# Kernel tuning notes

Measured on AMD Instinct MI355X. Metric: run time of the kernel, lower is better.

## Reference

```python
import jax, jax.numpy as jnp
import numpy as np
from jax import lax

SIM_THRESH = 0.9
MOTION_SCALE = 0.5
SALIENCY_SCALE = 0.5
EPS = 1e-6


def setup_inputs() -> dict:
    key = jax.random.key(0)
    k1, k2, k3, k4 = jax.random.split(key, 4)
    B, N, D, H, W = 128, 196, 768, 14, 14
    return {
        "tokens": jax.random.normal(k1, (B, N, D), dtype=jnp.float32),
        "motion_magnitude": jax.random.uniform(k2, (B, 1, H, W), dtype=jnp.float32),
        "saliency_map": jax.random.uniform(k3, (B, 1, H, W), dtype=jnp.float32),
        "compression_ratio": jax.random.uniform(k4, (B, H, W), dtype=jnp.float32),
    }


def _importance(motion, saliency, ratio):
    # motion/saliency are already (B,1,14,14) == (height,width), so
    # adaptive_avg_pool2d to (14,14) is the identity.
    B = motion.shape[0]
    m = motion.reshape(B, -1)
    m = m / (jnp.max(m) + EPS)               # global max, as in torch .max()
    s = saliency.reshape(B, -1)
    s = s / (jnp.max(s) + EPS)
    r = ratio.reshape(B, -1)
    imp = (MOTION_SCALE * m + SALIENCY_SCALE * s
           + (1.0 - MOTION_SCALE - SALIENCY_SCALE) * r)
    lo = imp.min(axis=1, keepdims=True)
    hi = imp.max(axis=1, keepdims=True)
    return (imp - lo) / (hi - lo + EPS)      # (B, N)


def _groups(adj):
    """Sequential BFS grouping over roots, faithful to the torch loop.

    adj: bool (N,N) directed edge mask. Returns (group_ids int32 (N,), num_groups).
    """
    N = adj.shape[0]

    def root_step(carry, r):
        assigned, gids, gid = carry

        def assign(c):
            assigned, gids, gid = c
            # BFS from root r, only through currently-unassigned nodes
            allowed = (~assigned).at[r].set(True)
            reach0 = jnp.zeros(N, dtype=bool).at[r].set(True)

            def body(s):
                reach, _ = s
                nxt = reach | (jnp.any(adj & reach[:, None], axis=0) & allowed)
                return nxt, jnp.any(nxt != reach)

            reach, _ = lax.while_loop(lambda s: s[1], body, (reach0, True))
            return assigned | reach, jnp.where(reach, gid, gids), gid + 1

        carry = lax.cond(assigned[r], lambda c: c, assign, carry)
        return carry, None

    init = (jnp.zeros(N, dtype=bool), jnp.zeros(N, dtype=jnp.int32), jnp.int32(0))
    (_, gids, ngroups), _ = lax.scan(root_step, init, jnp.arange(N))
    return gids, ngroups


def _merge_one(tokens_b, imp_b, adj_b):
    N = tokens_b.shape[0]
    gids, ng = _groups(adj_b)
    denom = jax.ops.segment_sum(imp_b, gids, num_segments=N) + EPS
    w = imp_b / denom[gids]
    merged = jax.ops.segment_sum(tokens_b * w[:, None], gids, num_segments=N)
    return merged, gids, ng


def reference(tokens, motion_magnitude, saliency_map, compression_ratio):
    B, N, D = tokens.shape
    imp = _importance(motion_magnitude, saliency_map, compression_ratio)  # (B,N)

    # cosine similarity (F.normalize with eps=1e-12)
    norm = jnp.maximum(jnp.linalg.norm(tokens, axis=-1, keepdims=True), 1e-12)
    tn = tokens / norm
    sim = jnp.einsum('bnd,bmd->bnm', tn, tn)
    sim = sim * (1.0 - jnp.eye(N, dtype=sim.dtype))  # zero diagonal

    # directed merge mask: similarity * (1 - importance_row)
    mask = (sim > SIM_THRESH).astype(sim.dtype) * (1.0 - imp[:, :, None])
    adj = mask > 0.5

    merged, gids, ng = jax.vmap(_merge_one)(tokens, imp, adj)
    # merged padded to N groups (rows >= num_groups are zero)
    return merged, sim, imp, gids
```

## Files before the change

### kernel.cpp

```cpp
#include <hip/hip_runtime.h>
#include <cstdint>

static constexpr int cB = 128;
static constexpr int cN = 196;
static constexpr int cD = 768;
static constexpr int cNN = cN * cN;
static constexpr int cND = cN * cD;
static constexpr float cEPS = 1e-6f;
static constexpr size_t cBND = (size_t)cB * cN * cD;

typedef __attribute__((ext_vector_type(8))) short short8;
typedef __attribute__((ext_vector_type(8))) unsigned short u16x8;
typedef __attribute__((ext_vector_type(4))) float f32x4;
typedef unsigned long long u64;

__device__ __forceinline__ unsigned short bf16_rne(float x) {
    unsigned u = __builtin_bit_cast(unsigned, x);
    u += 0x7FFFu + ((u >> 16) & 1u);
    return (unsigned short)(u >> 16);
}

__global__ __launch_bounds__(256) void k_imp(const float* __restrict__ mo,
                                             const float* __restrict__ sa,
                                             float* __restrict__ out_imp,
                                             float* __restrict__ ws_imp,
                                             float* __restrict__ ws_w,
                                             u64* __restrict__ ws_adj) {
    int b = blockIdx.x, t = threadIdx.x;
    __shared__ float redm[4], reds[4], lo_s[4], hi_s[4], MS[2], LOHI[2];

    for (int i = b * 256 + t; i < cB * cN * 4; i += cB * 256) ws_adj[i] = 0ull;

    const float4* mo4 = (const float4*)mo;
    const float4* sa4 = (const float4*)sa;
    float mm = 0.f, ms = 0.f;
    for (int i = t; i < cB * cN / 4; i += 256) {
        float4 a = mo4[i], c = sa4[i];
        mm = fmaxf(mm, fmaxf(fmaxf(a.x, a.y), fmaxf(a.z, a.w)));
        ms = fmaxf(ms, fmaxf(fmaxf(c.x, c.y), fmaxf(c.z, c.w)));
    }
    #pragma unroll
    for (int off = 32; off; off >>= 1) {
        mm = fmaxf(mm, __shfl_down(mm, off));
        ms = fmaxf(ms, __shfl_down(ms, off));
    }
    if ((t & 63) == 0) { redm[t >> 6] = mm; reds[t >> 6] = ms; }
    __syncthreads();
    if (t == 0) {
        float a = redm[0], c = reds[0];
        for (int w = 1; w < 4; w++) { a = fmaxf(a, redm[w]); c = fmaxf(c, reds[w]); }
        MS[0] = 1.0f / (a + cEPS);
        MS[1] = 1.0f / (c + cEPS);
    }
    __syncthreads();
    float Minv = MS[0], Sinv = MS[1];
    float v = 0.f, lo = 1e30f, hi = -1e30f;
    if (t < cN) {
        v = 0.5f * mo[b * cN + t] * Minv + 0.5f * sa[b * cN + t] * Sinv;
        lo = v; hi = v;
    }
    #pragma unroll
    for (int off = 32; off; off >>= 1) {
        lo = fminf(lo, __shfl_down(lo, off));
        hi = fmaxf(hi, __shfl_down(hi, off));
    }
    if ((t & 63) == 0) { lo_s[t >> 6] = lo; hi_s[t >> 6] = hi; }
    __syncthreads();
    if (t == 0) {
        float l = lo_s[0], h = hi_s[0];
        for (int w = 1; w < 4; w++) { l = fminf(l, lo_s[w]); h = fmaxf(h, hi_s[w]); }
        LOHI[0] = l; LOHI[1] = h;
    }
    __syncthreads();
    if (t < cN) {
        float imp = (v - LOHI[0]) / (LOHI[1] - LOHI[0] + cEPS);
        out_imp[b * cN + t] = imp;
        ws_imp[b * cN + t] = imp;
        ws_w[b * cN + t] = imp / (imp + cEPS);
    }
}

__global__ __launch_bounds__(256) void k_prep(const float* __restrict__ tok,
                                              const float* __restrict__ ws_w,
                                              float* __restrict__ ws_invn,
                                              float* __restrict__ merged) {
    int t = threadIdx.x;
    int tk = blockIdx.x * 8 + (t >> 5);
    int l  = t & 31;
    const float4* src = (const float4*)(tok + (size_t)tk * cD) + l;
    float4* dst = (float4*)(merged + (size_t)tk * cD) + l;
    float w = ws_w[tk];
    float4 v[6];
    #pragma unroll
    for (int j = 0; j < 6; j++) v[j] = src[32 * j];
    float s = 0.f;
    #pragma unroll
    for (int j = 0; j < 6; j++) {
        float4 x = v[j];
        s += x.x * x.x + x.y * x.y + x.z * x.z + x.w * x.w;
        dst[32 * j] = make_float4(x.x * w, x.y * w, x.z * w, x.w * w);
    }
    s += __shfl_xor(s, 1);  s += __shfl_xor(s, 2);
    s += __shfl_xor(s, 4);  s += __shfl_xor(s, 8);
    s += __shfl_xor(s, 16);
    if (l == 0) ws_invn[tk] = 1.0f / fmaxf(sqrtf(s), 1e-12f);
}

__global__ __launch_bounds__(256, 2) void k_sim(const float* __restrict__ tok,
                                                const float* __restrict__ ws_invn,
                                                const float* __restrict__ ws_imp,
                                                float* __restrict__ out_sim,
                                                u64* __restrict__ ws_adj) {
    __shared__ unsigned short sA[128 * 40];
    __shared__ unsigned short sB[128 * 40];
    __shared__ float invR[128], invC[128], impR[128];
    __shared__ u64 ldsAdj[256];

    int bid = blockIdx.x;
    int xcd = bid & 7;
    int lin = bid >> 3;
    int b   = xcd + 8 * (lin >> 2);
    int tile = lin & 3;
    int rb = (tile >> 1) * 128, cb = (tile & 1) * 128;

    int t = threadIdx.x;
    int w = t >> 6, lane = t & 63;
    int lr = lane & 15, kf = (lane >> 4) * 8;
    int wr = (w >> 1) * 64, wc = (w & 1) * 64;
    const size_t bN = (size_t)b * cN;
    const float* tb = tok + bN * cD;

    ldsAdj[t] = 0ull;
    if (t < 128) {
        int gr = rb + t;
        invR[t] = (gr < cN) ? ws_invn[bN + gr] : 0.f;
        impR[t] = (gr < cN) ? ws_imp[bN + gr] : 1.f;
    } else {
        int gc = cb + (t - 128);
        invC[t - 128] = (gc < cN) ? ws_invn[bN + gc] : 0.f;
    }

    f32x4 acc[4][4];
    #pragma unroll
    for (int i = 0; i < 4; i++)
        #pragma unroll
        for (int j = 0; j < 4; j++) acc[i][j] = (f32x4){0.f, 0.f, 0.f, 0.f};

    int srow = t >> 2;
    int q = t & 3;

    for (int k0 = 0; k0 < cD; k0 += 32) {
        #pragma unroll
        for (int p = 0; p < 2; ++p) {
            int row = srow + 64 * p;
            int koff = k0 + 8 * q;
            float4 a0 = make_float4(0.f, 0.f, 0.f, 0.f), a1 = a0;
            float4 b0 = a0, b1 = a0;
            int gr = rb + row;
            if (gr < cN) {
                const float4* pa = (const float4*)(tb + (size_t)gr * cD + koff);
                a0 = pa[0]; a1 = pa[1];
            }
            int gc = cb + row;
            if (gc < cN) {
                const float4* pb = (const float4*)(tb + (size_t)gc * cD + koff);
                b0 = pb[0]; b1 = pb[1];
            }
            u16x8 ha, hb;
            ha[0] = bf16_rne(a0.x); ha[1] = bf16_rne(a0.y);
            ha[2] = bf16_rne(a0.z); ha[3] = bf16_rne(a0.w);
            ha[4] = bf16_rne(a1.x); ha[5] = bf16_rne(a1.y);
            ha[6] = bf16_rne(a1.z); ha[7] = bf16_rne(a1.w);
            hb[0] = bf16_rne(b0.x); hb[1] = bf16_rne(b0.y);
            hb[2] = bf16_rne(b0.z); hb[3] = bf16_rne(b0.w);
            hb[4] = bf16_rne(b1.x); hb[5] = bf16_rne(b1.y);
            hb[6] = bf16_rne(b1.z); hb[7] = bf16_rne(b1.w);
            *(u16x8*)&sA[row * 40 + 8 * q] = ha;
            *(u16x8*)&sB[row * 40 + 8 * q] = hb;
        }
        __syncthreads();

        short8 af[4], bf[4];
        #pragma unroll
        for (int rg = 0; rg < 4; rg++)
            af[rg] = *(const short8*)&sA[(wr + 16 * rg + lr) * 40 + kf];
        #pragma unroll
        for (int cg = 0; cg < 4; cg++)
            bf[cg] = *(const short8*)&sB[(wc + 16 * cg + lr) * 40 + kf];
        #pragma unroll
        for (int rg = 0; rg < 4; rg++)
            #pragma unroll
            for (int cg = 0; cg < 4; cg++)
                acc[rg][cg] = __builtin_amdgcn_mfma_f32_16x16x32_bf16(af[rg], bf[cg], acc[rg][cg], 0, 0, 0);
        __syncthreads();
    }

    float* so = out_sim + (size_t)b * cNN;
    int wloc = w >> 1;
    #pragma unroll
    for (int rg = 0; rg < 4; rg++) {
        int rBaseLoc = wr + 16 * rg + (lane >> 4) * 4;
        #pragma unroll
        for (int cg = 0; cg < 4; cg++) {
            int cLoc = wc + 16 * cg + lr;
            int C = cb + cLoc;
            if (C >= cN) continue;
            float ic = invC[cLoc];
            u64 bits = 0ull;
            #pragma unroll
            for (int i = 0; i < 4; i++) {
                int rLoc = rBaseLoc + i;
                int R = rb + rLoc;
                if (R >= cN) continue;
                float val = (R == C) ? 0.f : acc[rg][cg][i] * invR[rLoc] * ic;
                so[(size_t)R * cN + C] = val;
                if (val > 0.9f && impR[rLoc] < 0.5f) bits |= 1ull << (R & 63);
            }
            if (bits) atomicOr(&ldsAdj[cLoc * 2 + wloc], bits);
        }
    }
    __syncthreads();
    {
        int cLoc = t >> 1, wl = t & 1;
        int C = cb + cLoc;
        u64 v = ldsAdj[t];
        if (C < cN && v)
            atomicOr(&ws_adj[((size_t)b * cN + C) * 4 + (rb >> 6) + wl], v);
    }
}

__global__ __launch_bounds__(256) void k_group(const u64* __restrict__ ws_adj,
                                               const float* __restrict__ ws_imp,
                                               const float* __restrict__ tok,
                                               float* __restrict__ out_gids,
                                               float* __restrict__ ws_w,
                                               int* __restrict__ ws_flag,
                                               int* __restrict__ ws_gids,
                                               float* __restrict__ merged) {
    int b = blockIdx.x, t = threadIdx.x;
    __shared__ float impL[cN];
    __shared__ u64 reachw[4], assignedw[4], edge_s[4];
    __shared__ int flag;
    __shared__ int gidsL[cN];
    __shared__ float denomL[cN];
    __shared__ float wL[cN];

    u64 m0 = 0, m1 = 0, m2 = 0, m3 = 0;
    if (t < cN) {
        impL[t] = ws_imp[b * cN + t];
        const u64* ap = ws_adj + ((size_t)b * cN + t) * 4;
        m0 = ap[0]; m1 = ap[1]; m2 = ap[2]; m3 = ap[3];
    }
    u64 anym = m0 | m1 | m2 | m3;
    u64 bal = __ballot(anym != 0ull);
    if ((t & 63) == 0) edge_s[t >> 6] = bal;
    __syncthreads();
    bool has_edges = (edge_s[0] | edge_s[1] | edge_s[2] | edge_s[3]) != 0ull;

    if (!has_edges) {
        if (t < cN) {
            float imp = impL[t];
            ws_w[b * cN + t] = imp / (imp + cEPS);
            ws_gids[b * cN + t] = t;
            out_gids[b * cN + t] = (float)t;
        }
        if (t == 0) ws_flag[b] = 1;
        return;
    }

    if (t < 4) assignedw[t] = 0ull;
    if (t < cN) { gidsL[t] = 0; denomL[t] = 0.f; }
    __syncthreads();
    int gid = 0;
    int wrd_t = t >> 6, bit_t = t & 63;
    for (int r = 0; r < cN; r++) {
        if ((assignedw[r >> 6] >> (r & 63)) & 1ull) continue;
        if (t < 4) reachw[t] = (t == (r >> 6)) ? (1ull << (r & 63)) : 0ull;
        __syncthreads();
        int changed = 1;
        while (changed) {
            u64 hit = (m0 & reachw[0]) | (m1 & reachw[1]) |
                      (m2 & reachw[2]) | (m3 & reachw[3]);
            bool inre = (t < cN) && ((reachw[wrd_t] >> bit_t) & 1ull);
            bool unass = (t < cN) && !((assignedw[wrd_t] >> bit_t) & 1ull);
            bool p = inre || (hit != 0ull && unass);
            u64 nw = __ballot(p);
            __syncthreads();
            if (t == 0) flag = 0;
            __syncthreads();
            if ((t & 63) == 0) {
                if (nw != reachw[t >> 6]) flag = 1;
                reachw[t >> 6] = nw;
            }
            __syncthreads();
            changed = flag;
        }
        if ((t < cN) && ((reachw[wrd_t] >> bit_t) & 1ull)) gidsL[t] = gid;
        if (t < 4) assignedw[t] |= reachw[t];
        gid++;
        __syncthreads();
    }
    if (t < cN) atomicAdd(&denomL[gidsL[t]], impL[t]);
    __syncthreads();
    if (t < cN) {
        int g = gidsL[t];
        float wv = impL[t] / (denomL[g] + cEPS);
        ws_w[b * cN + t] = wv;
        wL[t] = wv;
        ws_gids[b * cN + t] = g;
        out_gids[b * cN + t] = (float)g;
    }
    if (t == 0) ws_flag[b] = 0;
    __syncthreads();

    if (t < 192) {
        for (int n = 0; n < cN; n++) {
            float4 acc = make_float4(0.f, 0.f, 0.f, 0.f);
            for (int j = 0; j < cN; j++) {
                if (gidsL[j] == n) {
                    const float4 v = *(const float4*)(tok + (size_t)b * cND + (size_t)j * cD + 4 * t);
                    float wv = wL[j];
                    acc.x += v.x * wv; acc.y += v.y * wv;
                    acc.z += v.z * wv; acc.w += v.w * wv;
                }
            }
            *(float4*)(merged + (size_t)b * cND + (size_t)n * cD + 4 * t) = acc;
        }
    }
}

extern "C" void kernel_launch(void* const* d_in, const int* in_sizes, int n_in,
                              void* d_out, int out_size, void* d_ws, size_t ws_size,
                              hipStream_t stream) {
    const float* tok = (const float*)d_in[0];
    const float* mo  = (const float*)d_in[1];
    const float* sa  = (const float*)d_in[2];

    float* out = (float*)d_out;
    float* out_merged = out;
    float* out_sim    = out + cBND;
    float* out_imp    = out_sim + (size_t)cB * cNN;
    float* out_gids   = out_imp + (size_t)cB * cN;

    u64*   ws_adj  = (u64*)d_ws;
    float* ws_imp  = (float*)(ws_adj + (size_t)cB * cN * 4);
    float* ws_w    = ws_imp + cB * cN;
    float* ws_invn = ws_w + cB * cN;
    int*   ws_flag = (int*)(ws_invn + cB * cN);
    int*   ws_gids = ws_flag + cB;

    k_imp<<<cB, 256, 0, stream>>>(mo, sa, out_imp, ws_imp, ws_w, ws_adj);
    k_prep<<<cB * cN / 8, 256, 0, stream>>>(tok, ws_w, ws_invn, out_merged);
    k_sim<<<512, 256, 0, stream>>>(tok, ws_invn, ws_imp, out_sim, ws_adj);
    k_group<<<cB, 256, 0, stream>>>(ws_adj, ws_imp, tok, out_gids, ws_w,
                                    ws_flag, ws_gids, out_merged);
}
```

Baseline: 218.8 us.

## Exploit similarity symmetry to compute three tiles per batch and prefetch loads

The similarity kernel now computes only the two diagonal tiles and one off-diagonal tile per batch, mirroring the off-diagonal results into the transposed output and adjacency bits. Diagonal tiles reuse the A shared buffer for both operands, which skips the B loads. The K loop is also software-pipelined, with register double buffers prefetching the next slice of global loads while the MFMAs run. In exchange, the off-diagonal block writes transposed, uncoalesced stores, issues per-element LDS atomics, and holds more registers.

```diff
diff --git a/kernel.cpp b/kernel.cpp
--- a/kernel.cpp
+++ b/kernel.cpp
@@ -113,15 +113,18 @@
                                                 u64* __restrict__ ws_adj) {
     __shared__ unsigned short sA[128 * 40];
     __shared__ unsigned short sB[128 * 40];
-    __shared__ float invR[128], invC[128], impR[128];
+    __shared__ float invR[128], invC[128], impR[128], impC[128];
     __shared__ u64 ldsAdj[256];
+    __shared__ u64 ldsAdjT[256];
 
     int bid = blockIdx.x;
     int xcd = bid & 7;
     int lin = bid >> 3;
-    int b   = xcd + 8 * (lin >> 2);
-    int tile = lin & 3;
-    int rb = (tile >> 1) * 128, cb = (tile & 1) * 128;
+    int b   = xcd + 8 * (lin / 3);
+    int tc  = lin % 3;
+    int rb = (tc == 2) ? 128 : 0;
+    int cb = (tc == 0) ? 0 : 128;
+    bool diag = (tc != 1);
 
     int t = threadIdx.x;
     int w = t >> 6, lane = t & 63;
@@ -131,6 +134,7 @@
     const float* tb = tok + bN * cD;
 
     ldsAdj[t] = 0ull;
+    ldsAdjT[t] = 0ull;
     if (t < 128) {
         int gr = rb + t;
         invR[t] = (gr < cN) ? ws_invn[bN + gr] : 0.f;
@@ -138,6 +142,7 @@
     } else {
         int gc = cb + (t - 128);
         invC[t - 128] = (gc < cN) ? ws_invn[bN + gc] : 0.f;
+        impC[t - 128] = (gc < cN) ? ws_imp[bN + gc] : 1.f;
     }
 
     f32x4 acc[4][4];
@@ -149,49 +154,81 @@
     int srow = t >> 2;
     int q = t & 3;
 
-    for (int k0 = 0; k0 < cD; k0 += 32) {
+    float4 bufA[8], bufB[8];
+
+    auto LOADS = [&](int k0, float4 (&r)[8]) {
+        int koff = k0 + 8 * q;
         #pragma unroll
         for (int p = 0; p < 2; ++p) {
             int row = srow + 64 * p;
-            int koff = k0 + 8 * q;
-            float4 a0 = make_float4(0.f, 0.f, 0.f, 0.f), a1 = a0;
-            float4 b0 = a0, b1 = a0;
+            float4 z = make_float4(0.f, 0.f, 0.f, 0.f);
+            r[2 * p] = z; r[2 * p + 1] = z;
             int gr = rb + row;
             if (gr < cN) {
                 const float4* pa = (const float4*)(tb + (size_t)gr * cD + koff);
-                a0 = pa[0]; a1 = pa[1];
-            }
-            int gc = cb + row;
-            if (gc < cN) {
-                const float4* pb = (const float4*)(tb + (size_t)gc * cD + koff);
-                b0 = pb[0]; b1 = pb[1];
-            }
-            u16x8 ha, hb;
+                r[2 * p] = pa[0]; r[2 * p + 1] = pa[1];
+            }
+            if (!diag) {
+                r[4 + 2 * p] = z; r[4 + 2 * p + 1] = z;
+                int gc = cb + row;
+                if (gc < cN) {
+                    const float4* pb = (const float4*)(tb + (size_t)gc * cD + koff);
+                    r[4 + 2 * p] = pb[0]; r[4 + 2 * p + 1] = pb[1];
+                }
+            }
+        }
+    };
+    auto PACK = [&](const float4 (&r)[8]) {
+        #pragma unroll
+        for (int p = 0; p < 2; ++p) {
+            int row = srow + 64 * p;
+            float4 a0 = r[2 * p], a1 = r[2 * p + 1];
+            u16x8 ha;
             ha[0] = bf16_rne(a0.x); ha[1] = bf16_rne(a0.y);
             ha[2] = bf16_rne(a0.z); ha[3] = bf16_rne(a0.w);
             ha[4] = bf16_rne(a1.x); ha[5] = bf16_rne(a1.y);
             ha[6] = bf16_rne(a1.z); ha[7] = bf16_rne(a1.w);
-            hb[0] = bf16_rne(b0.x); hb[1] = bf16_rne(b0.y);
-            hb[2] = bf16_rne(b0.z); hb[3] = bf16_rne(b0.w);
-            hb[4] = bf16_rne(b1.x); hb[5] = bf16_rne(b1.y);
-            hb[6] = bf16_rne(b1.z); hb[7] = bf16_rne(b1.w);
             *(u16x8*)&sA[row * 40 + 8 * q] = ha;
-            *(u16x8*)&sB[row * 40 + 8 * q] = hb;
-        }
-        __syncthreads();
-
+            if (!diag) {
+                float4 b0 = r[4 + 2 * p], b1 = r[4 + 2 * p + 1];
+                u16x8 hb;
+                hb[0] = bf16_rne(b0.x); hb[1] = bf16_rne(b0.y);
+                hb[2] = bf16_rne(b0.z); hb[3] = bf16_rne(b0.w);
+                hb[4] = bf16_rne(b1.x); hb[5] = bf16_rne(b1.y);
+                hb[6] = bf16_rne(b1.z); hb[7] = bf16_rne(b1.w);
+                *(u16x8*)&sB[row * 40 + 8 * q] = hb;
+            }
+        }
+    };
+    auto COMPUTE = [&]() {
         short8 af[4], bf[4];
         #pragma unroll
         for (int rg = 0; rg < 4; rg++)
             af[rg] = *(const short8*)&sA[(wr + 16 * rg + lr) * 40 + kf];
+        const unsigned short* sS = diag ? sA : sB;
         #pragma unroll
         for (int cg = 0; cg < 4; cg++)
-            bf[cg] = *(const short8*)&sB[(wc + 16 * cg + lr) * 40 + kf];
+            bf[cg] = *(const short8*)&sS[(wc + 16 * cg + lr) * 40 + kf];
         #pragma unroll
         for (int rg = 0; rg < 4; rg++)
             #pragma unroll
             for (int cg = 0; cg < 4; cg++)
-                acc[rg][cg] = __builtin_amdgcn_mfma_f32_16x16x32_bf16(af[rg], bf[cg], acc[rg][cg], 0, 0, 0);
+                acc[rg][cg] = __builtin_amdgcn_mfma_f32_16x16x32_bf16(
+                    af[rg], bf[cg], acc[rg][cg], 0, 0, 0);
+    };
+
+    LOADS(0, bufA);
+    for (int k0 = 0; k0 < cD; k0 += 64) {
+        PACK(bufA);
+        __syncthreads();
+        LOADS(k0 + 32, bufB);
+        COMPUTE();
+        __syncthreads();
+
+        PACK(bufB);
+        __syncthreads();
+        if (k0 + 64 < cD) LOADS(k0 + 64, bufA);
+        COMPUTE();
         __syncthreads();
     }
 
@@ -206,6 +243,7 @@
             int C = cb + cLoc;
             if (C >= cN) continue;
             float ic = invC[cLoc];
+            float imC = impC[cLoc];
             u64 bits = 0ull;
             #pragma unroll
             for (int i = 0; i < 4; i++) {
@@ -215,6 +253,12 @@
                 float val = (R == C) ? 0.f : acc[rg][cg][i] * invR[rLoc] * ic;
                 so[(size_t)R * cN + C] = val;
                 if (val > 0.9f && impR[rLoc] < 0.5f) bits |= 1ull << (R & 63);
+                if (!diag) {
+                    so[(size_t)C * cN + R] = val;
+                    if (val > 0.9f && imC < 0.5f)
+                        atomicOr(&ldsAdjT[rLoc * 2 + ((C >> 6) & 1)],
+                                 1ull << (C & 63));
+                }
             }
             if (bits) atomicOr(&ldsAdj[cLoc * 2 + wloc], bits);
         }
@@ -226,6 +270,11 @@
         u64 v = ldsAdj[t];
         if (C < cN && v)
             atomicOr(&ws_adj[((size_t)b * cN + C) * 4 + (rb >> 6) + wl], v);
+        if (!diag) {
+            u64 vt = ldsAdjT[t];
+            if (vt)
+                atomicOr(&ws_adj[((size_t)b * cN + cLoc) * 4 + 2 + wl], vt);
+        }
     }
 }
 
@@ -351,7 +400,7 @@
 
     k_imp<<<cB, 256, 0, stream>>>(mo, sa, out_imp, ws_imp, ws_w, ws_adj);
     k_prep<<<cB * cN / 8, 256, 0, stream>>>(tok, ws_w, ws_invn, out_merged);
-    k_sim<<<512, 256, 0, stream>>>(tok, ws_invn, ws_imp, out_sim, ws_adj);
+    k_sim<<<384, 256, 0, stream>>>(tok, ws_invn, ws_imp, out_sim, ws_adj);
     k_group<<<cB, 256, 0, stream>>>(ws_adj, ws_imp, tok, out_gids, ws_w,
                                     ws_flag, ws_gids, out_merged);
 }
```

After: 212.5 us. -2.9%, faster.
